# Kernel optimization log

Measured on AMD Instinct MI355X. Metric: run time of the kernel, lower is better.

Reference implementation:

```python
import jax, jax.numpy as jnp
import numpy as np
from functools import partial

H = 64  # hidden_size
F = 5   # num_features
ALPHA_RANK = 1.0
NEG_SLOPE = 0.2


def setup_inputs() -> dict:
    key = jax.random.key(0)
    ks = jax.random.split(key, 10)
    N, T = 4096, 512
    feature = jax.random.normal(ks[0], (N, T, F), dtype=jnp.float32)
    ret = jax.random.normal(ks[1], (N,), dtype=jnp.float32)
    mask = jax.random.bernoulli(ks[2], 0.9, (N,))
    s = 1.0 / np.sqrt(H)
    Wih = jax.random.uniform(ks[3], (4 * H, F), jnp.float32, -s, s)
    Whh = jax.random.uniform(ks[4], (4 * H, H), jnp.float32, -s, s)
    bih = jax.random.uniform(ks[5], (4 * H,), jnp.float32, -s, s)
    bhh = jax.random.uniform(ks[6], (4 * H,), jnp.float32, -s, s)
    Wd = jax.random.uniform(ks[7], (1, H), jnp.float32, -s, s)
    bd = jax.random.uniform(ks[8], (1,), jnp.float32, -s, s)
    return {"feature": feature, "ret": ret, "mask": mask,
            "Wih": Wih, "Whh": Whh, "bih": bih, "bhh": bhh,
            "Wd": Wd, "bd": bd}


def _lstm_last_h(x, Wih, Whh, bih, bhh):
    # x: [N, T, F] -> last hidden state [N, H]. PyTorch gate order: i, f, g, o.
    N = x.shape[0]
    b = bih + bhh
    # precompute input projections for all steps: [T, N, 4H]
    x_proj = jnp.einsum('ntf,gf->tng', x, Wih) + b

    def step(carry, xt):
        h, c = carry
        gates = xt + h @ Whh.T  # [N, 4H]
        i, f, g, o = jnp.split(gates, 4, axis=-1)
        i = jax.nn.sigmoid(i)
        f = jax.nn.sigmoid(f)
        g = jnp.tanh(g)
        o = jax.nn.sigmoid(o)
        c = f * c + i * g
        h = o * jnp.tanh(c)
        return (h, c), None

    h0 = jnp.zeros((N, H), x.dtype)
    c0 = jnp.zeros((N, H), x.dtype)
    (h, _), _ = jax.lax.scan(step, (h0, c0), x_proj)
    return h


def _masked_mse(pred, gt, mask):
    m = mask.astype(pred.dtype)
    return jnp.sum((pred - gt) ** 2 * m) / (jnp.sum(m) + 1e-8)


def _rank_loss(pred, gt, mask):
    m = mask.astype(pred.dtype)
    pred_diff = pred[None, :] - pred[:, None]   # [i,j] = pred[j]-pred[i]
    true_diff = gt[None, :] - gt[:, None]
    mm = m[None, :] * m[:, None]
    return jnp.mean(jax.nn.relu(-pred_diff * true_diff * mm))


def reference(feature, ret, mask, Wih, Whh, bih, bhh, Wd, bd):
    h_last = _lstm_last_h(feature, Wih, Whh, bih, bhh)          # [N, H]
    pred = jax.nn.leaky_relu(h_last @ Wd.T + bd, NEG_SLOPE)[:, 0]  # [N]
    reg_loss = _masked_mse(pred, ret, mask)
    rank_loss = _rank_loss(pred, ret, mask)
    loss = reg_loss + ALPHA_RANK * rank_loss
    return pred, loss, reg_loss, rank_loss
```

## Files before the change

kernel.cpp:

```cpp
#include <hip/hip_runtime.h>

#define NSEQ   4096
#define TSTEPS 512
#define FIN    5
#define HID    64
#define SPB    16
#define BLK    512

typedef __attribute__((ext_vector_type(8))) short bsh8;
typedef __attribute__((ext_vector_type(4))) float f32x4;
typedef __attribute__((ext_vector_type(2))) float f32x2;
typedef __attribute__((ext_vector_type(4))) int   i32x4;

#define MFMA16(A, B, C) __builtin_amdgcn_mfma_f32_16x16x32_bf16((A), (B), (C), 0, 0, 0)

#define LOG2E 1.4426950408889634f
#define SNEG  (-LOG2E)
#define SPOS  (2.0f * LOG2E)

struct Frag2 { bsh8 hi; bsh8 lo; };

__device__ __forceinline__ unsigned short bf16hi_rn(float x) {
    unsigned u = __float_as_uint(x);
    return (unsigned short)((u + 0x7fffu + ((u >> 16) & 1u)) >> 16);
}
__device__ __forceinline__ void split_bf16(float v, unsigned short& h, unsigned short& l) {
    h = bf16hi_rn(v);
    float hf_ = __uint_as_float(((unsigned)h) << 16);
    l = bf16hi_rn(v - hf_);
}

__device__ __forceinline__ Frag2 load_whh_frag(const float* __restrict__ Whh, int row, int k, float scale) {
    const float* p = Whh + row * HID + k;
    Frag2 r;
#pragma unroll
    for (int j = 0; j < 8; ++j) {
        unsigned short h, l;
        split_bf16(scale * p[j], h, l);
        r.hi[j] = (short)h; r.lo[j] = (short)l;
    }
    return r;
}
__device__ __forceinline__ Frag2 load_wih_frag(const float* __restrict__ Wih,
                                               const float* __restrict__ bih,
                                               const float* __restrict__ bhh,
                                               int row, int quad, float scale) {
    Frag2 r;
#pragma unroll
    for (int j = 0; j < 8; ++j) { r.hi[j] = 0; r.lo[j] = 0; }
    if (quad == 0) {
        unsigned short h, l;
#pragma unroll
        for (int j = 0; j < FIN; ++j) {
            split_bf16(scale * Wih[row * FIN + j], h, l);
            r.hi[j] = (short)h; r.lo[j] = (short)l;
        }
        split_bf16(scale * (bih[row] + bhh[row]), h, l);
        r.hi[FIN] = (short)h; r.lo[FIN] = (short)l;
    }
    return r;
}

__device__ __forceinline__ void stage_chunk(const float* __restrict__ feat,
                                            bsh8 (*dst)[SPB],
                                            int seq0, int t0, int tidE) {
#pragma unroll
    for (int it = 0; it < (64 * SPB) / 256; ++it) {
        int idx = tidE + it * 256;
        int t2  = idx >> 4;
        int s   = idx & 15;
        const float* xp = feat + (size_t)(seq0 + s) * (TSTEPS * FIN) + (t0 + t2) * FIN;
        bsh8 v = {0, 0, 0, 0, 0, 0, 0, 0};
#pragma unroll
        for (int j = 0; j < FIN; ++j) v[j] = (short)bf16hi_rn(xp[j]);
        v[FIN] = (short)0x3F80;
        dst[t2][s] = v;
    }
}

__device__ __forceinline__ void epi2(float zi0, float zf0, float zg0, float zo0,
                                     float zi1, float zf1, float zg1, float zo1,
                                     float& cs0, float& cs1, float& h0, float& h1) {
    float Ei0 = __builtin_amdgcn_exp2f(zi0), Ei1 = __builtin_amdgcn_exp2f(zi1);
    float Ef0 = __builtin_amdgcn_exp2f(zf0), Ef1 = __builtin_amdgcn_exp2f(zf1);
    float Eg0 = __builtin_amdgcn_exp2f(zg0), Eg1 = __builtin_amdgcn_exp2f(zg1);
    float P10 = (1.0f + Ei0) * (1.0f + Eg0), Pf0 = 1.0f + Ef0;
    float P11 = (1.0f + Ei1) * (1.0f + Eg1), Pf1 = 1.0f + Ef1;
    float D0 = P10 * Pf0, D1 = P11 * Pf1;
    float Rp = __builtin_amdgcn_rcpf(D0 * D1);
    float n10 = __builtin_fmaf(SPOS, Eg0, -SPOS);
    float n11 = __builtin_fmaf(SPOS, Eg1, -SPOS);
    float m0 = __builtin_fmaf(P10, cs0, n10 * Pf0);
    float m1 = __builtin_fmaf(P11, cs1, n11 * Pf1);
    cs0 = (Rp * D1) * m0;
    cs1 = (Rp * D0) * m1;
    float Eo0 = __builtin_amdgcn_exp2f(zo0), Eo1 = __builtin_amdgcn_exp2f(zo1);
    float Ec0 = __builtin_amdgcn_exp2f(cs0), Ec1 = __builtin_amdgcn_exp2f(cs1);
    float D20 = (1.0f + Eo0) * (1.0f + Ec0);
    float D21 = (1.0f + Eo1) * (1.0f + Ec1);
    float R2p = __builtin_amdgcn_rcpf(D20 * D21);
    h0 = (Ec0 - 1.0f) * (R2p * D21);
    h1 = (Ec1 - 1.0f) * (R2p * D20);
}

__global__ __launch_bounds__(BLK)
void lstm_kernel(const float* __restrict__ feat,
                 const float* __restrict__ Wih,
                 const float* __restrict__ Whh,
                 const float* __restrict__ bih,
                 const float* __restrict__ bhh,
                 const float* __restrict__ Wd,
                 const float* __restrict__ bd,
                 float* __restrict__ pred,
                 float* __restrict__ accums) {
    __shared__ bsh8  aA[2][SPB][9];
    __shared__ bsh8  xb[2][64][SPB];
    __shared__ __align__(8) f32x2 sg[2][4][4][64];
    __shared__ __align__(8) f32x2 mb[4][4][64];
    __shared__ float hf[SPB][HID + 1];
    __shared__ float pf[SPB][17];

    const int tid   = threadIdx.x;
    const int w     = tid >> 6;
    const int lane  = tid & 63;
    const int col   = lane & 15;
    const int quad  = lane >> 4;
    const int quad4 = quad * 4;
    const int seq0  = blockIdx.x * SPB;

    if (blockIdx.x == 0 && tid < 4) accums[tid] = 0.0f;

    {
        bsh8 z = {0, 0, 0, 0, 0, 0, 0, 0};
        if (tid < SPB * 9) (&aA[0][0][0])[tid] = z;
    }
    if (w >= 4) stage_chunk(feat, xb[0], seq0, 0, tid - 256);
    __syncthreads();

    if (w < 4) {
        const int u = 16 * w + col;
        const Frag2 b00 = load_whh_frag(Whh, 0*HID + u,      quad*8, SNEG);
        const Frag2 b01 = load_whh_frag(Whh, 0*HID + u, 32 + quad*8, SNEG);
        const Frag2 b10 = load_whh_frag(Whh, 1*HID + u,      quad*8, SNEG);
        const Frag2 b11 = load_whh_frag(Whh, 1*HID + u, 32 + quad*8, SNEG);
        const Frag2 b20 = load_whh_frag(Whh, 2*HID + u,      quad*8, SPOS);
        const Frag2 b21 = load_whh_frag(Whh, 2*HID + u, 32 + quad*8, SPOS);
        const Frag2 b30 = load_whh_frag(Whh, 3*HID + u,      quad*8, SNEG);
        const Frag2 b31 = load_whh_frag(Whh, 3*HID + u, 32 + quad*8, SNEG);

        float cs0 = 0.f, cs1 = 0.f;
        unsigned short* const aAb = (unsigned short*)&aA[0][0][0];
        const int rowbase = quad4 * 72 + u;
        const int aAhalf  = SPB * 9 * 8;

        for (int t = 0; t < TSTEPS; ++t) {
            const int buf = t & 1;
            const int nb  = buf ^ 1;
            __builtin_amdgcn_s_setprio(1);
            __syncthreads();

            bsh8 ah0 = aA[buf][col][quad];
            bsh8 ah1 = aA[buf][col][4 + quad];
            f32x2 s0 = sg[buf][w][0][lane];
            f32x2 s1 = sg[buf][w][1][lane];
            f32x2 s2 = sg[buf][w][2][lane];
            f32x2 s3 = sg[buf][w][3][lane];

            const f32x4 zz = {0.f, 0.f, 0.f, 0.f};
            f32x4 acc0 = MFMA16(ah0, b00.hi, zz);
            f32x4 acc1 = MFMA16(ah0, b10.hi, zz);
            f32x4 acc2 = MFMA16(ah0, b20.hi, zz);
            f32x4 acc3 = MFMA16(ah0, b30.hi, zz);
            acc0 = MFMA16(ah1, b01.hi, acc0);
            acc1 = MFMA16(ah1, b11.hi, acc1);
            acc2 = MFMA16(ah1, b21.hi, acc2);
            acc3 = MFMA16(ah1, b31.hi, acc3);
            acc0 = MFMA16(ah0, b00.lo, acc0);
            acc1 = MFMA16(ah0, b10.lo, acc1);
            acc2 = MFMA16(ah0, b20.lo, acc2);
            acc3 = MFMA16(ah0, b30.lo, acc3);
            acc0 = MFMA16(ah1, b01.lo, acc0);
            acc1 = MFMA16(ah1, b11.lo, acc1);
            acc2 = MFMA16(ah1, b21.lo, acc2);
            acc3 = MFMA16(ah1, b31.lo, acc3);

            mb[w][0][lane] = (f32x2){acc0[2], acc0[3]};
            mb[w][1][lane] = (f32x2){acc1[2], acc1[3]};
            mb[w][2][lane] = (f32x2){acc2[2], acc2[3]};
            mb[w][3][lane] = (f32x2){acc3[2], acc3[3]};
            __builtin_amdgcn_s_setprio(0);
            __syncthreads();

            float h0, h1;
            epi2(acc0[0] + s0.x, acc1[0] + s1.x, acc2[0] + s2.x, acc3[0] + s3.x,
                 acc0[1] + s0.y, acc1[1] + s1.y, acc2[1] + s2.y, acc3[1] + s3.y,
                 cs0, cs1, h0, h1);
            unsigned pk;
            asm("v_cvt_pk_bf16_f32 %0, %1, %2" : "=v"(pk) : "v"(h0), "v"(h1));
            unsigned short* hp = aAb + nb * aAhalf + rowbase;
            hp[0]  = (unsigned short)pk;
            hp[72] = (unsigned short)(pk >> 16);
            if (t == TSTEPS - 1) {
                hf[quad4 + 0][u] = h0;
                hf[quad4 + 1][u] = h1;
            }
        }
    } else {
        const int wE   = w - 4;
        const int tidE = tid - 256;
        const int uE   = 16 * wE + col;
        const Frag2 w0 = load_wih_frag(Wih, bih, bhh, 0*HID + uE, quad, SNEG);
        const Frag2 w1 = load_wih_frag(Wih, bih, bhh, 1*HID + uE, quad, SNEG);
        const Frag2 w2 = load_wih_frag(Wih, bih, bhh, 2*HID + uE, quad, SPOS);
        const Frag2 w3 = load_wih_frag(Wih, bih, bhh, 3*HID + uE, quad, SNEG);

        float cs2 = 0.f, cs3 = 0.f;
        f32x2 ps0, ps1, ps2, ps3;
        unsigned short* const aAb = (unsigned short*)&aA[0][0][0];
        const int rowbase = (quad4 + 2) * 72 + uE;
        const int aAhalf  = SPB * 9 * 8;

        {
            bsh8 ax = xb[0][0][col];
            f32x4 e0 = {0.f,0.f,0.f,0.f}, e1 = e0, e2 = e0, e3 = e0;
            e0 = MFMA16(ax, w0.hi, e0); e0 = MFMA16(ax, w0.lo, e0);
            e1 = MFMA16(ax, w1.hi, e1); e1 = MFMA16(ax, w1.lo, e1);
            e2 = MFMA16(ax, w2.hi, e2); e2 = MFMA16(ax, w2.lo, e2);
            e3 = MFMA16(ax, w3.hi, e3); e3 = MFMA16(ax, w3.lo, e3);
            sg[0][wE][0][lane] = (f32x2){e0[0], e0[1]};
            sg[0][wE][1][lane] = (f32x2){e1[0], e1[1]};
            sg[0][wE][2][lane] = (f32x2){e2[0], e2[1]};
            sg[0][wE][3][lane] = (f32x2){e3[0], e3[1]};
            ps0 = (f32x2){e0[2], e0[3]};
            ps1 = (f32x2){e1[2], e1[3]};
            ps2 = (f32x2){e2[2], e2[3]};
            ps3 = (f32x2){e3[2], e3[3]};
        }

        for (int t = 0; t < TSTEPS; ++t) {
            const int nb = (t & 1) ^ 1;
            __syncthreads();
            f32x2 ns0, ns1, ns2, ns3;
            bool have_ns = (t + 1 < TSTEPS);
            if ((t & 63) == 0 && t + 64 < TSTEPS)
                stage_chunk(feat, xb[((t >> 6) + 1) & 1], seq0, ((t >> 6) + 1) * 64, tidE);
            if (have_ns) {
                const int t1 = t + 1;
                bsh8 ax = xb[(t1 >> 6) & 1][t1 & 63][col];
                f32x4 e0 = {0.f,0.f,0.f,0.f}, e1 = e0, e2 = e0, e3 = e0;
                e0 = MFMA16(ax, w0.hi, e0); e0 = MFMA16(ax, w0.lo, e0);
                e1 = MFMA16(ax, w1.hi, e1); e1 = MFMA16(ax, w1.lo, e1);
                e2 = MFMA16(ax, w2.hi, e2); e2 = MFMA16(ax, w2.lo, e2);
                e3 = MFMA16(ax, w3.hi, e3); e3 = MFMA16(ax, w3.lo, e3);
                sg[nb][wE][0][lane] = (f32x2){e0[0], e0[1]};
                sg[nb][wE][1][lane] = (f32x2){e1[0], e1[1]};
                sg[nb][wE][2][lane] = (f32x2){e2[0], e2[1]};
                sg[nb][wE][3][lane] = (f32x2){e3[0], e3[1]};
                ns0 = (f32x2){e0[2], e0[3]};
                ns1 = (f32x2){e1[2], e1[3]};
                ns2 = (f32x2){e2[2], e2[3]};
                ns3 = (f32x2){e3[2], e3[3]};
            }
            __syncthreads();

            f32x2 m0 = mb[wE][0][lane];
            f32x2 m1 = mb[wE][1][lane];
            f32x2 m2 = mb[wE][2][lane];
            f32x2 m3 = mb[wE][3][lane];
            float h2, h3;
            epi2(m0.x + ps0.x, m1.x + ps1.x, m2.x + ps2.x, m3.x + ps3.x,
                 m0.y + ps0.y, m1.y + ps1.y, m2.y + ps2.y, m3.y + ps3.y,
                 cs2, cs3, h2, h3);
            unsigned pk;
            asm("v_cvt_pk_bf16_f32 %0, %1, %2" : "=v"(pk) : "v"(h2), "v"(h3));
            unsigned short* hp = aAb + nb * aAhalf + rowbase;
            hp[0]  = (unsigned short)pk;
            hp[72] = (unsigned short)(pk >> 16);
            if (have_ns) { ps0 = ns0; ps1 = ns1; ps2 = ns2; ps3 = ns3; }
            else {
                hf[quad4 + 2][uE] = h2;
                hf[quad4 + 3][uE] = h3;
            }
        }
    }
    __syncthreads();

    if (tid < 256) {
        int s  = tid & 15;
        int hq = tid >> 4;
        int j0 = hq * 4;
        float part = hf[s][j0] * Wd[j0] + hf[s][j0 + 1] * Wd[j0 + 1]
                   + hf[s][j0 + 2] * Wd[j0 + 2] + hf[s][j0 + 3] * Wd[j0 + 3];
        pf[s][hq] = part;
    }
    __syncthreads();
    if (tid < SPB) {
        float sum = bd[0];
#pragma unroll
        for (int j = 0; j < 16; ++j) sum += pf[tid][j];
        float p = (sum >= 0.0f) ? sum : 0.2f * sum;
        pred[seq0 + tid] = p;
    }
}

__global__ __launch_bounds__(256)
void loss_kernel(const float* __restrict__ pred,
                 const float* __restrict__ ret,
                 const int* __restrict__ mask,
                 float* __restrict__ accums) {
    __shared__ __align__(16) float sp[NSEQ];
    __shared__ __align__(16) float sg_[NSEQ];
    __shared__ __align__(16) float sq[NSEQ];
    __shared__ float wsum[8];
    int tid = threadIdx.x;
    for (int idx = tid; idx < NSEQ / 4; idx += 256) {
        f32x4 p4 = ((const f32x4*)pred)[idx];
        f32x4 g4 = ((const f32x4*)ret)[idx];
        i32x4 m4 = ((const i32x4*)mask)[idx];
        f32x4 q4;
#pragma unroll
        for (int l = 0; l < 4; ++l) q4[l] = m4[l] ? 1.0f : 0.0f;
        *(f32x4*)&sp[idx * 4] = p4;
        *(f32x4*)&sg_[idx * 4] = g4;
        *(f32x4*)&sq[idx * 4] = q4;
    }
    __syncthreads();

    if (blockIdx.x == 0) {
        float v = 0.0f, m = 0.0f;
        for (int j = tid; j < NSEQ; j += 256) {
            float mj = sq[j];
            float d  = sp[j] - sg_[j];
            v += d * d * mj;
            m += mj;
        }
#pragma unroll
        for (int off = 32; off > 0; off >>= 1) {
            v += __shfl_down(v, off, 64);
            m += __shfl_down(m, off, 64);
        }
        if ((tid & 63) == 0) {
            atomicAdd(&accums[0], v);
            atomicAdd(&accums[1], m);
        }
    }

    int iloc = tid >> 5;
    int jp   = tid & 31;
    int i    = blockIdx.x * 8 + iloc;
    float pi = sp[i], gi = sg_[i], qi = sq[i];
    float sum = 0.0f;
    for (int j0 = jp * 4; j0 < NSEQ; j0 += 128) {
        f32x4 p4 = *(const f32x4*)&sp[j0];
        f32x4 g4 = *(const f32x4*)&sg_[j0];
        f32x4 q4 = *(const f32x4*)&sq[j0];
#pragma unroll
        for (int l = 0; l < 4; ++l) {
            float t = -(p4[l] - pi) * (g4[l] - gi);
            sum += fmaxf(t, 0.0f) * q4[l];
        }
    }
    sum *= qi;
#pragma unroll
    for (int off = 16; off > 0; off >>= 1) sum += __shfl_down(sum, off, 32);
    if (jp == 0) wsum[iloc] = sum;
    __syncthreads();
    if (tid == 0) {
        float s = wsum[0] + wsum[1] + wsum[2] + wsum[3]
                + wsum[4] + wsum[5] + wsum[6] + wsum[7];
        atomicAdd(&accums[2], s);
    }
}

__global__ void final_kernel(const float* __restrict__ accums,
                             float* __restrict__ out) {
    float reg  = accums[0] / (accums[1] + 1e-8f);
    float rank = accums[2] / 16777216.0f;
    out[NSEQ + 0] = reg + rank;
    out[NSEQ + 1] = reg;
    out[NSEQ + 2] = rank;
}

extern "C" void kernel_launch(void* const* d_in, const int* in_sizes, int n_in,
                              void* d_out, int out_size, void* d_ws, size_t ws_size,
                              hipStream_t stream) {
    const float* feat = (const float*)d_in[0];
    const float* ret  = (const float*)d_in[1];
    const int*   mask = (const int*)d_in[2];
    const float* Wih  = (const float*)d_in[3];
    const float* Whh  = (const float*)d_in[4];
    const float* bih  = (const float*)d_in[5];
    const float* bhh  = (const float*)d_in[6];
    const float* Wd   = (const float*)d_in[7];
    const float* bd   = (const float*)d_in[8];
    float* out    = (float*)d_out;
    float* accums = (float*)d_ws;

    lstm_kernel<<<NSEQ / SPB, BLK, 0, stream>>>(feat, Wih, Whh, bih, bhh,
                                                Wd, bd, out, accums);
    loss_kernel<<<NSEQ / 8, 256, 0, stream>>>(out, ret, mask, accums);
    final_kernel<<<1, 1, 0, stream>>>(accums, out);
}
```

Measured before the change: 412.3 us.

## Merge producer and recurrent waves to halve per-step barriers via redundant MFMA

Replaces the warp-specialised split, where four waves ran the recurrent MFMAs and four ran input projection plus half the gate epilogue, with a uniform scheme. Every wave now computes the full recurrent and input-projection MFMAs redundantly and keeps only its half of the output rows. This removes the sg/mb LDS exchange buffers and one __syncthreads per time step, shortening the serial critical path of the recurrence. The cost is roughly double the MFMA work per SIMD, and the s_setprio hints are dropped.

```diff
diff --git a/kernel.cpp b/kernel.cpp
--- a/kernel.cpp
+++ b/kernel.cpp
@@ -63,10 +63,10 @@
 
 __device__ __forceinline__ void stage_chunk(const float* __restrict__ feat,
                                             bsh8 (*dst)[SPB],
-                                            int seq0, int t0, int tidE) {
-#pragma unroll
-    for (int it = 0; it < (64 * SPB) / 256; ++it) {
-        int idx = tidE + it * 256;
+                                            int seq0, int t0, int tid) {
+#pragma unroll
+    for (int it = 0; it < (64 * SPB) / BLK; ++it) {
+        int idx = tid + it * BLK;
         int t2  = idx >> 4;
         int s   = idx & 15;
         const float* xp = feat + (size_t)(seq0 + s) * (TSTEPS * FIN) + (t0 + t2) * FIN;
@@ -115,8 +115,6 @@
                  float* __restrict__ accums) {
     __shared__ bsh8  aA[2][SPB][9];
     __shared__ bsh8  xb[2][64][SPB];
-    __shared__ __align__(8) f32x2 sg[2][4][4][64];
-    __shared__ __align__(8) f32x2 mb[4][4][64];
     __shared__ float hf[SPB][HID + 1];
     __shared__ float pf[SPB][17];
 
@@ -126,6 +124,10 @@
     const int col   = lane & 15;
     const int quad  = lane >> 4;
     const int quad4 = quad * 4;
+    const int wg    = w & 3;
+    const int half  = w >> 2;
+    const int u     = 16 * wg + col;
+    const int r0    = quad4 + 2 * half;
     const int seq0  = blockIdx.x * SPB;
 
     if (blockIdx.x == 0 && tid < 4) accums[tid] = 0.0f;
@@ -134,153 +136,103 @@
         bsh8 z = {0, 0, 0, 0, 0, 0, 0, 0};
         if (tid < SPB * 9) (&aA[0][0][0])[tid] = z;
     }
-    if (w >= 4) stage_chunk(feat, xb[0], seq0, 0, tid - 256);
-    __syncthreads();
-
-    if (w < 4) {
-        const int u = 16 * w + col;
-        const Frag2 b00 = load_whh_frag(Whh, 0*HID + u,      quad*8, SNEG);
-        const Frag2 b01 = load_whh_frag(Whh, 0*HID + u, 32 + quad*8, SNEG);
-        const Frag2 b10 = load_whh_frag(Whh, 1*HID + u,      quad*8, SNEG);
-        const Frag2 b11 = load_whh_frag(Whh, 1*HID + u, 32 + quad*8, SNEG);
-        const Frag2 b20 = load_whh_frag(Whh, 2*HID + u,      quad*8, SPOS);
-        const Frag2 b21 = load_whh_frag(Whh, 2*HID + u, 32 + quad*8, SPOS);
-        const Frag2 b30 = load_whh_frag(Whh, 3*HID + u,      quad*8, SNEG);
-        const Frag2 b31 = load_whh_frag(Whh, 3*HID + u, 32 + quad*8, SNEG);
-
-        float cs0 = 0.f, cs1 = 0.f;
-        unsigned short* const aAb = (unsigned short*)&aA[0][0][0];
-        const int rowbase = quad4 * 72 + u;
-        const int aAhalf  = SPB * 9 * 8;
-
-        for (int t = 0; t < TSTEPS; ++t) {
-            const int buf = t & 1;
-            const int nb  = buf ^ 1;
-            __builtin_amdgcn_s_setprio(1);
-            __syncthreads();
-
-            bsh8 ah0 = aA[buf][col][quad];
-            bsh8 ah1 = aA[buf][col][4 + quad];
-            f32x2 s0 = sg[buf][w][0][lane];
-            f32x2 s1 = sg[buf][w][1][lane];
-            f32x2 s2 = sg[buf][w][2][lane];
-            f32x2 s3 = sg[buf][w][3][lane];
-
-            const f32x4 zz = {0.f, 0.f, 0.f, 0.f};
-            f32x4 acc0 = MFMA16(ah0, b00.hi, zz);
-            f32x4 acc1 = MFMA16(ah0, b10.hi, zz);
-            f32x4 acc2 = MFMA16(ah0, b20.hi, zz);
-            f32x4 acc3 = MFMA16(ah0, b30.hi, zz);
-            acc0 = MFMA16(ah1, b01.hi, acc0);
-            acc1 = MFMA16(ah1, b11.hi, acc1);
-            acc2 = MFMA16(ah1, b21.hi, acc2);
-            acc3 = MFMA16(ah1, b31.hi, acc3);
-            acc0 = MFMA16(ah0, b00.lo, acc0);
-            acc1 = MFMA16(ah0, b10.lo, acc1);
-            acc2 = MFMA16(ah0, b20.lo, acc2);
-            acc3 = MFMA16(ah0, b30.lo, acc3);
-            acc0 = MFMA16(ah1, b01.lo, acc0);
-            acc1 = MFMA16(ah1, b11.lo, acc1);
-            acc2 = MFMA16(ah1, b21.lo, acc2);
-            acc3 = MFMA16(ah1, b31.lo, acc3);
-
-            mb[w][0][lane] = (f32x2){acc0[2], acc0[3]};
-            mb[w][1][lane] = (f32x2){acc1[2], acc1[3]};
-            mb[w][2][lane] = (f32x2){acc2[2], acc2[3]};
-            mb[w][3][lane] = (f32x2){acc3[2], acc3[3]};
-            __builtin_amdgcn_s_setprio(0);
-            __syncthreads();
-
-            float h0, h1;
-            epi2(acc0[0] + s0.x, acc1[0] + s1.x, acc2[0] + s2.x, acc3[0] + s3.x,
-                 acc0[1] + s0.y, acc1[1] + s1.y, acc2[1] + s2.y, acc3[1] + s3.y,
-                 cs0, cs1, h0, h1);
-            unsigned pk;
-            asm("v_cvt_pk_bf16_f32 %0, %1, %2" : "=v"(pk) : "v"(h0), "v"(h1));
-            unsigned short* hp = aAb + nb * aAhalf + rowbase;
-            hp[0]  = (unsigned short)pk;
-            hp[72] = (unsigned short)(pk >> 16);
-            if (t == TSTEPS - 1) {
-                hf[quad4 + 0][u] = h0;
-                hf[quad4 + 1][u] = h1;
-            }
-        }
-    } else {
-        const int wE   = w - 4;
-        const int tidE = tid - 256;
-        const int uE   = 16 * wE + col;
-        const Frag2 w0 = load_wih_frag(Wih, bih, bhh, 0*HID + uE, quad, SNEG);
-        const Frag2 w1 = load_wih_frag(Wih, bih, bhh, 1*HID + uE, quad, SNEG);
-        const Frag2 w2 = load_wih_frag(Wih, bih, bhh, 2*HID + uE, quad, SPOS);
-        const Frag2 w3 = load_wih_frag(Wih, bih, bhh, 3*HID + uE, quad, SNEG);
-
-        float cs2 = 0.f, cs3 = 0.f;
-        f32x2 ps0, ps1, ps2, ps3;
-        unsigned short* const aAb = (unsigned short*)&aA[0][0][0];
-        const int rowbase = (quad4 + 2) * 72 + uE;
-        const int aAhalf  = SPB * 9 * 8;
-
-        {
-            bsh8 ax = xb[0][0][col];
+    stage_chunk(feat, xb[0], seq0, 0, tid);
+
+    const Frag2 b00 = load_whh_frag(Whh, 0*HID + u,      quad*8, SNEG);
+    const Frag2 b01 = load_whh_frag(Whh, 0*HID + u, 32 + quad*8, SNEG);
+    const Frag2 b10 = load_whh_frag(Whh, 1*HID + u,      quad*8, SNEG);
+    const Frag2 b11 = load_whh_frag(Whh, 1*HID + u, 32 + quad*8, SNEG);
+    const Frag2 b20 = load_whh_frag(Whh, 2*HID + u,      quad*8, SPOS);
+    const Frag2 b21 = load_whh_frag(Whh, 2*HID + u, 32 + quad*8, SPOS);
+    const Frag2 b30 = load_whh_frag(Whh, 3*HID + u,      quad*8, SNEG);
+    const Frag2 b31 = load_whh_frag(Whh, 3*HID + u, 32 + quad*8, SNEG);
+    const Frag2 w0_ = load_wih_frag(Wih, bih, bhh, 0*HID + u, quad, SNEG);
+    const Frag2 w1_ = load_wih_frag(Wih, bih, bhh, 1*HID + u, quad, SNEG);
+    const Frag2 w2_ = load_wih_frag(Wih, bih, bhh, 2*HID + u, quad, SPOS);
+    const Frag2 w3_ = load_wih_frag(Wih, bih, bhh, 3*HID + u, quad, SNEG);
+
+    __syncthreads();
+
+    float cs0 = 0.f, cs1 = 0.f;
+    f32x2 ps0, ps1, ps2, ps3;
+
+    {
+        bsh8 ax = xb[0][0][col];
+        f32x4 e0 = {0.f,0.f,0.f,0.f}, e1 = e0, e2 = e0, e3 = e0;
+        e0 = MFMA16(ax, w0_.hi, e0); e0 = MFMA16(ax, w0_.lo, e0);
+        e1 = MFMA16(ax, w1_.hi, e1); e1 = MFMA16(ax, w1_.lo, e1);
+        e2 = MFMA16(ax, w2_.hi, e2); e2 = MFMA16(ax, w2_.lo, e2);
+        e3 = MFMA16(ax, w3_.hi, e3); e3 = MFMA16(ax, w3_.lo, e3);
+        ps0 = half ? (f32x2){e0[2], e0[3]} : (f32x2){e0[0], e0[1]};
+        ps1 = half ? (f32x2){e1[2], e1[3]} : (f32x2){e1[0], e1[1]};
+        ps2 = half ? (f32x2){e2[2], e2[3]} : (f32x2){e2[0], e2[1]};
+        ps3 = half ? (f32x2){e3[2], e3[3]} : (f32x2){e3[0], e3[1]};
+    }
+
+    unsigned short* const aAb = (unsigned short*)&aA[0][0][0];
+    const int rowbase = r0 * 72 + u;
+    const int aAhalf  = SPB * 9 * 8;
+
+    for (int t = 0; t < TSTEPS; ++t) {
+        const int buf = t & 1;
+        const int nb  = buf ^ 1;
+        __syncthreads();
+
+        bsh8 ah0 = aA[buf][col][quad];
+        bsh8 ah1 = aA[buf][col][4 + quad];
+
+        const f32x4 zz = {0.f, 0.f, 0.f, 0.f};
+        f32x4 acc0 = MFMA16(ah0, b00.hi, zz);
+        f32x4 acc1 = MFMA16(ah0, b10.hi, zz);
+        f32x4 acc2 = MFMA16(ah0, b20.hi, zz);
+        f32x4 acc3 = MFMA16(ah0, b30.hi, zz);
+        acc0 = MFMA16(ah1, b01.hi, acc0);
+        acc1 = MFMA16(ah1, b11.hi, acc1);
+        acc2 = MFMA16(ah1, b21.hi, acc2);
+        acc3 = MFMA16(ah1, b31.hi, acc3);
+        acc0 = MFMA16(ah0, b00.lo, acc0);
+        acc1 = MFMA16(ah0, b10.lo, acc1);
+        acc2 = MFMA16(ah0, b20.lo, acc2);
+        acc3 = MFMA16(ah0, b30.lo, acc3);
+        acc0 = MFMA16(ah1, b01.lo, acc0);
+        acc1 = MFMA16(ah1, b11.lo, acc1);
+        acc2 = MFMA16(ah1, b21.lo, acc2);
+        acc3 = MFMA16(ah1, b31.lo, acc3);
+
+        float a00 = half ? acc0[2] : acc0[0], a01 = half ? acc0[3] : acc0[1];
+        float a10 = half ? acc1[2] : acc1[0], a11 = half ? acc1[3] : acc1[1];
+        float a20 = half ? acc2[2] : acc2[0], a21 = half ? acc2[3] : acc2[1];
+        float a30 = half ? acc3[2] : acc3[0], a31 = half ? acc3[3] : acc3[1];
+
+        float h0, h1;
+        epi2(a00 + ps0.x, a10 + ps1.x, a20 + ps2.x, a30 + ps3.x,
+             a01 + ps0.y, a11 + ps1.y, a21 + ps2.y, a31 + ps3.y,
+             cs0, cs1, h0, h1);
+
+        unsigned pk;
+        asm("v_cvt_pk_bf16_f32 %0, %1, %2" : "=v"(pk) : "v"(h0), "v"(h1));
+        unsigned short* hp = aAb + nb * aAhalf + rowbase;
+        hp[0]  = (unsigned short)pk;
+        hp[72] = (unsigned short)(pk >> 16);
+        if (t == TSTEPS - 1) {
+            hf[r0 + 0][u] = h0;
+            hf[r0 + 1][u] = h1;
+        }
+
+        if ((t & 63) == 0 && t + 64 < TSTEPS)
+            stage_chunk(feat, xb[((t >> 6) + 1) & 1], seq0, ((t >> 6) + 1) * 64, tid);
+        if (t + 1 < TSTEPS) {
+            const int t1 = t + 1;
+            bsh8 ax = xb[(t1 >> 6) & 1][t1 & 63][col];
             f32x4 e0 = {0.f,0.f,0.f,0.f}, e1 = e0, e2 = e0, e3 = e0;
-            e0 = MFMA16(ax, w0.hi, e0); e0 = MFMA16(ax, w0.lo, e0);
-            e1 = MFMA16(ax, w1.hi, e1); e1 = MFMA16(ax, w1.lo, e1);
-            e2 = MFMA16(ax, w2.hi, e2); e2 = MFMA16(ax, w2.lo, e2);
-            e3 = MFMA16(ax, w3.hi, e3); e3 = MFMA16(ax, w3.lo, e3);
-            sg[0][wE][0][lane] = (f32x2){e0[0], e0[1]};
-            sg[0][wE][1][lane] = (f32x2){e1[0], e1[1]};
-            sg[0][wE][2][lane] = (f32x2){e2[0], e2[1]};
-            sg[0][wE][3][lane] = (f32x2){e3[0], e3[1]};
-            ps0 = (f32x2){e0[2], e0[3]};
-            ps1 = (f32x2){e1[2], e1[3]};
-            ps2 = (f32x2){e2[2], e2[3]};
-            ps3 = (f32x2){e3[2], e3[3]};
-        }
-
-        for (int t = 0; t < TSTEPS; ++t) {
-            const int nb = (t & 1) ^ 1;
-            __syncthreads();
-            f32x2 ns0, ns1, ns2, ns3;
-            bool have_ns = (t + 1 < TSTEPS);
-            if ((t & 63) == 0 && t + 64 < TSTEPS)
-                stage_chunk(feat, xb[((t >> 6) + 1) & 1], seq0, ((t >> 6) + 1) * 64, tidE);
-            if (have_ns) {
-                const int t1 = t + 1;
-                bsh8 ax = xb[(t1 >> 6) & 1][t1 & 63][col];
-                f32x4 e0 = {0.f,0.f,0.f,0.f}, e1 = e0, e2 = e0, e3 = e0;
-                e0 = MFMA16(ax, w0.hi, e0); e0 = MFMA16(ax, w0.lo, e0);
-                e1 = MFMA16(ax, w1.hi, e1); e1 = MFMA16(ax, w1.lo, e1);
-                e2 = MFMA16(ax, w2.hi, e2); e2 = MFMA16(ax, w2.lo, e2);
-                e3 = MFMA16(ax, w3.hi, e3); e3 = MFMA16(ax, w3.lo, e3);
-                sg[nb][wE][0][lane] = (f32x2){e0[0], e0[1]};
-                sg[nb][wE][1][lane] = (f32x2){e1[0], e1[1]};
-                sg[nb][wE][2][lane] = (f32x2){e2[0], e2[1]};
-                sg[nb][wE][3][lane] = (f32x2){e3[0], e3[1]};
-                ns0 = (f32x2){e0[2], e0[3]};
-                ns1 = (f32x2){e1[2], e1[3]};
-                ns2 = (f32x2){e2[2], e2[3]};
-                ns3 = (f32x2){e3[2], e3[3]};
-            }
-            __syncthreads();
-
-            f32x2 m0 = mb[wE][0][lane];
-            f32x2 m1 = mb[wE][1][lane];
-            f32x2 m2 = mb[wE][2][lane];
-            f32x2 m3 = mb[wE][3][lane];
-            float h2, h3;
-            epi2(m0.x + ps0.x, m1.x + ps1.x, m2.x + ps2.x, m3.x + ps3.x,
-                 m0.y + ps0.y, m1.y + ps1.y, m2.y + ps2.y, m3.y + ps3.y,
-                 cs2, cs3, h2, h3);
-            unsigned pk;
-            asm("v_cvt_pk_bf16_f32 %0, %1, %2" : "=v"(pk) : "v"(h2), "v"(h3));
-            unsigned short* hp = aAb + nb * aAhalf + rowbase;
-            hp[0]  = (unsigned short)pk;
-            hp[72] = (unsigned short)(pk >> 16);
-            if (have_ns) { ps0 = ns0; ps1 = ns1; ps2 = ns2; ps3 = ns3; }
-            else {
-                hf[quad4 + 2][uE] = h2;
-                hf[quad4 + 3][uE] = h3;
-            }
+            e0 = MFMA16(ax, w0_.hi, e0); e0 = MFMA16(ax, w0_.lo, e0);
+            e1 = MFMA16(ax, w1_.hi, e1); e1 = MFMA16(ax, w1_.lo, e1);
+            e2 = MFMA16(ax, w2_.hi, e2); e2 = MFMA16(ax, w2_.lo, e2);
+            e3 = MFMA16(ax, w3_.hi, e3); e3 = MFMA16(ax, w3_.lo, e3);
+            ps0 = half ? (f32x2){e0[2], e0[3]} : (f32x2){e0[0], e0[1]};
+            ps1 = half ? (f32x2){e1[2], e1[3]} : (f32x2){e1[0], e1[1]};
+            ps2 = half ? (f32x2){e2[2], e2[3]} : (f32x2){e2[0], e2[1]};
+            ps3 = half ? (f32x2){e3[2], e3[3]} : (f32x2){e3[0], e3[1]};
         }
     }
     __syncthreads();
```

Result: slower. 432.7 us (+5.0%).

## Halve sequences per block and drop mid-step barrier via lane shuffles

Applied to the files above, without the earlier changes.

Sequences per block drop from 16 to 8, so there are twice as many blocks, and the MFMA tiles keep 16 columns with the unused half zero-padded. The recurrent warps now take the upper accumulator rows from the opposite half-wave with __shfl_xor and run the whole gate epilogue themselves. That removes the LDS handoff buffer, the second per-step __syncthreads, and the epilogue work the input-projection warps used to do. The cost is that half of the MFMA work computes padding, and each block now covers fewer sequences for the same per-step latency. Launch bounds now request 4 blocks to raise occupancy.

```diff
diff --git a/kernel.cpp b/kernel.cpp
--- a/kernel.cpp
+++ b/kernel.cpp
@@ -4,7 +4,7 @@
 #define TSTEPS 512
 #define FIN    5
 #define HID    64
-#define SPB    16
+#define SPB    8
 #define BLK    512
 
 typedef __attribute__((ext_vector_type(8))) short bsh8;
@@ -62,13 +62,13 @@
 }
 
 __device__ __forceinline__ void stage_chunk(const float* __restrict__ feat,
-                                            bsh8 (*dst)[SPB],
+                                            bsh8 (*dst)[16],
                                             int seq0, int t0, int tidE) {
 #pragma unroll
     for (int it = 0; it < (64 * SPB) / 256; ++it) {
         int idx = tidE + it * 256;
-        int t2  = idx >> 4;
-        int s   = idx & 15;
+        int t2  = idx >> 3;
+        int s   = idx & 7;
         const float* xp = feat + (size_t)(seq0 + s) * (TSTEPS * FIN) + (t0 + t2) * FIN;
         bsh8 v = {0, 0, 0, 0, 0, 0, 0, 0};
 #pragma unroll
@@ -103,7 +103,7 @@
     h1 = (Ec1 - 1.0f) * (R2p * D20);
 }
 
-__global__ __launch_bounds__(BLK)
+__global__ __launch_bounds__(BLK, 4)
 void lstm_kernel(const float* __restrict__ feat,
                  const float* __restrict__ Wih,
                  const float* __restrict__ Whh,
@@ -113,10 +113,9 @@
                  const float* __restrict__ bd,
                  float* __restrict__ pred,
                  float* __restrict__ accums) {
-    __shared__ bsh8  aA[2][SPB][9];
-    __shared__ bsh8  xb[2][64][SPB];
+    __shared__ bsh8  aA[2][16][9];
+    __shared__ bsh8  xb[2][64][16];
     __shared__ __align__(8) f32x2 sg[2][4][4][64];
-    __shared__ __align__(8) f32x2 mb[4][4][64];
     __shared__ float hf[SPB][HID + 1];
     __shared__ float pf[SPB][17];
 
@@ -125,17 +124,26 @@
     const int lane  = tid & 63;
     const int col   = lane & 15;
     const int quad  = lane >> 4;
-    const int quad4 = quad * 4;
     const int seq0  = blockIdx.x * SPB;
 
     if (blockIdx.x == 0 && tid < 4) accums[tid] = 0.0f;
 
     {
         bsh8 z = {0, 0, 0, 0, 0, 0, 0, 0};
-        if (tid < SPB * 9) (&aA[0][0][0])[tid] = z;
+        if (tid < 2 * 16 * 9) (&aA[0][0][0])[tid] = z;
+#pragma unroll
+        for (int k = 0; k < 2; ++k) {
+            int i  = tid + k * BLK;
+            int b  = i >> 9;
+            int t2 = (i >> 3) & 63;
+            int s8 = 8 + (i & 7);
+            xb[b][t2][s8] = z;
+        }
     }
     if (w >= 4) stage_chunk(feat, xb[0], seq0, 0, tid - 256);
-    __syncthreads();
+
+    const int rA  = (quad & 1) * 4 + ((quad >> 1) ? 2 : 0);
+    const bool loq = (quad < 2);
 
     if (w < 4) {
         const int u = 16 * w + col;
@@ -148,15 +156,17 @@
         const Frag2 b30 = load_whh_frag(Whh, 3*HID + u,      quad*8, SNEG);
         const Frag2 b31 = load_whh_frag(Whh, 3*HID + u, 32 + quad*8, SNEG);
 
+        __syncthreads();
+
         float cs0 = 0.f, cs1 = 0.f;
         unsigned short* const aAb = (unsigned short*)&aA[0][0][0];
-        const int rowbase = quad4 * 72 + u;
-        const int aAhalf  = SPB * 9 * 8;
+        const int rowbase = rA * 72 + u;
+        const int aAhalf  = 16 * 9 * 8;
+        __builtin_amdgcn_s_setprio(1);
 
         for (int t = 0; t < TSTEPS; ++t) {
             const int buf = t & 1;
             const int nb  = buf ^ 1;
-            __builtin_amdgcn_s_setprio(1);
             __syncthreads();
 
             bsh8 ah0 = aA[buf][col][quad];
@@ -184,27 +194,28 @@
             acc2 = MFMA16(ah1, b21.lo, acc2);
             acc3 = MFMA16(ah1, b31.lo, acc3);
 
-            mb[w][0][lane] = (f32x2){acc0[2], acc0[3]};
-            mb[w][1][lane] = (f32x2){acc1[2], acc1[3]};
-            mb[w][2][lane] = (f32x2){acc2[2], acc2[3]};
-            mb[w][3][lane] = (f32x2){acc3[2], acc3[3]};
-            __builtin_amdgcn_s_setprio(0);
-            __syncthreads();
+            float x00 = __shfl_xor(acc0[2], 32, 64), x01 = __shfl_xor(acc0[3], 32, 64);
+            float x10 = __shfl_xor(acc1[2], 32, 64), x11 = __shfl_xor(acc1[3], 32, 64);
+            float x20 = __shfl_xor(acc2[2], 32, 64), x21 = __shfl_xor(acc2[3], 32, 64);
+            float x30 = __shfl_xor(acc3[2], 32, 64), x31 = __shfl_xor(acc3[3], 32, 64);
+            float zi0 = (loq ? acc0[0] : x00) + s0.x, zi1 = (loq ? acc0[1] : x01) + s0.y;
+            float zf0 = (loq ? acc1[0] : x10) + s1.x, zf1 = (loq ? acc1[1] : x11) + s1.y;
+            float zg0 = (loq ? acc2[0] : x20) + s2.x, zg1 = (loq ? acc2[1] : x21) + s2.y;
+            float zo0 = (loq ? acc3[0] : x30) + s3.x, zo1 = (loq ? acc3[1] : x31) + s3.y;
 
             float h0, h1;
-            epi2(acc0[0] + s0.x, acc1[0] + s1.x, acc2[0] + s2.x, acc3[0] + s3.x,
-                 acc0[1] + s0.y, acc1[1] + s1.y, acc2[1] + s2.y, acc3[1] + s3.y,
-                 cs0, cs1, h0, h1);
+            epi2(zi0, zf0, zg0, zo0, zi1, zf1, zg1, zo1, cs0, cs1, h0, h1);
             unsigned pk;
             asm("v_cvt_pk_bf16_f32 %0, %1, %2" : "=v"(pk) : "v"(h0), "v"(h1));
             unsigned short* hp = aAb + nb * aAhalf + rowbase;
             hp[0]  = (unsigned short)pk;
             hp[72] = (unsigned short)(pk >> 16);
             if (t == TSTEPS - 1) {
-                hf[quad4 + 0][u] = h0;
-                hf[quad4 + 1][u] = h1;
+                hf[rA + 0][u] = h0;
+                hf[rA + 1][u] = h1;
             }
         }
+        __builtin_amdgcn_s_setprio(0);
     } else {
         const int wE   = w - 4;
         const int tidE = tid - 256;
@@ -214,11 +225,7 @@
         const Frag2 w2 = load_wih_frag(Wih, bih, bhh, 2*HID + uE, quad, SPOS);
         const Frag2 w3 = load_wih_frag(Wih, bih, bhh, 3*HID + uE, quad, SNEG);
 
-        float cs2 = 0.f, cs3 = 0.f;
-        f32x2 ps0, ps1, ps2, ps3;
-        unsigned short* const aAb = (unsigned short*)&aA[0][0][0];
-        const int rowbase = (quad4 + 2) * 72 + uE;
-        const int aAhalf  = SPB * 9 * 8;
+        __syncthreads();
 
         {
             bsh8 ax = xb[0][0][col];
@@ -227,24 +234,20 @@
             e1 = MFMA16(ax, w1.hi, e1); e1 = MFMA16(ax, w1.lo, e1);
             e2 = MFMA16(ax, w2.hi, e2); e2 = MFMA16(ax, w2.lo, e2);
             e3 = MFMA16(ax, w3.hi, e3); e3 = MFMA16(ax, w3.lo, e3);
-            sg[0][wE][0][lane] = (f32x2){e0[0], e0[1]};
-            sg[0][wE][1][lane] = (f32x2){e1[0], e1[1]};
-            sg[0][wE][2][lane] = (f32x2){e2[0], e2[1]};
-            sg[0][wE][3][lane] = (f32x2){e3[0], e3[1]};
-            ps0 = (f32x2){e0[2], e0[3]};
-            ps1 = (f32x2){e1[2], e1[3]};
-            ps2 = (f32x2){e2[2], e2[3]};
-            ps3 = (f32x2){e3[2], e3[3]};
-        }
-
+            float x0 = __shfl_xor(e0[2], 32, 64), x0b = __shfl_xor(e0[3], 32, 64);
+            float x1 = __shfl_xor(e1[2], 32, 64), x1b = __shfl_xor(e1[3], 32, 64);
+            float x2 = __shfl_xor(e2[2], 32, 64), x2b = __shfl_xor(e2[3], 32, 64);
+            float x3 = __shfl_xor(e3[2], 32, 64), x3b = __shfl_xor(e3[3], 32, 64);
+            sg[0][wE][0][lane] = (f32x2){loq ? e0[0] : x0, loq ? e0[1] : x0b};
+            sg[0][wE][1][lane] = (f32x2){loq ? e1[0] : x1, loq ? e1[1] : x1b};
+            sg[0][wE][2][lane] = (f32x2){loq ? e2[0] : x2, loq ? e2[1] : x2b};
+            sg[0][wE][3][lane] = (f32x2){loq ? e3[0] : x3, loq ? e3[1] : x3b};
+        }
         for (int t = 0; t < TSTEPS; ++t) {
-            const int nb = (t & 1) ^ 1;
             __syncthreads();
-            f32x2 ns0, ns1, ns2, ns3;
-            bool have_ns = (t + 1 < TSTEPS);
             if ((t & 63) == 0 && t + 64 < TSTEPS)
                 stage_chunk(feat, xb[((t >> 6) + 1) & 1], seq0, ((t >> 6) + 1) * 64, tidE);
-            if (have_ns) {
+            if (t + 1 < TSTEPS) {
                 const int t1 = t + 1;
                 bsh8 ax = xb[(t1 >> 6) & 1][t1 & 63][col];
                 f32x4 e0 = {0.f,0.f,0.f,0.f}, e1 = e0, e2 = e0, e3 = e0;
@@ -252,42 +255,23 @@
                 e1 = MFMA16(ax, w1.hi, e1); e1 = MFMA16(ax, w1.lo, e1);
                 e2 = MFMA16(ax, w2.hi, e2); e2 = MFMA16(ax, w2.lo, e2);
                 e3 = MFMA16(ax, w3.hi, e3); e3 = MFMA16(ax, w3.lo, e3);
-                sg[nb][wE][0][lane] = (f32x2){e0[0], e0[1]};
-                sg[nb][wE][1][lane] = (f32x2){e1[0], e1[1]};
-                sg[nb][wE][2][lane] = (f32x2){e2[0], e2[1]};
-                sg[nb][wE][3][lane] = (f32x2){e3[0], e3[1]};
-                ns0 = (f32x2){e0[2], e0[3]};
-                ns1 = (f32x2){e1[2], e1[3]};
-                ns2 = (f32x2){e2[2], e2[3]};
-                ns3 = (f32x2){e3[2], e3[3]};
+                float x0 = __shfl_xor(e0[2], 32, 64), x0b = __shfl_xor(e0[3], 32, 64);
+                float x1 = __shfl_xor(e1[2], 32, 64), x1b = __shfl_xor(e1[3], 32, 64);
+                float x2 = __shfl_xor(e2[2], 32, 64), x2b = __shfl_xor(e2[3], 32, 64);
+                float x3 = __shfl_xor(e3[2], 32, 64), x3b = __shfl_xor(e3[3], 32, 64);
+                const int sb = t1 & 1;
+                sg[sb][wE][0][lane] = (f32x2){loq ? e0[0] : x0, loq ? e0[1] : x0b};
+                sg[sb][wE][1][lane] = (f32x2){loq ? e1[0] : x1, loq ? e1[1] : x1b};
+                sg[sb][wE][2][lane] = (f32x2){loq ? e2[0] : x2, loq ? e2[1] : x2b};
+                sg[sb][wE][3][lane] = (f32x2){loq ? e3[0] : x3, loq ? e3[1] : x3b};
             }
-            __syncthreads();
-
-            f32x2 m0 = mb[wE][0][lane];
-            f32x2 m1 = mb[wE][1][lane];
-            f32x2 m2 = mb[wE][2][lane];
-            f32x2 m3 = mb[wE][3][lane];
-            float h2, h3;
-            epi2(m0.x + ps0.x, m1.x + ps1.x, m2.x + ps2.x, m3.x + ps3.x,
-                 m0.y + ps0.y, m1.y + ps1.y, m2.y + ps2.y, m3.y + ps3.y,
-                 cs2, cs3, h2, h3);
-            unsigned pk;
-            asm("v_cvt_pk_bf16_f32 %0, %1, %2" : "=v"(pk) : "v"(h2), "v"(h3));
-            unsigned short* hp = aAb + nb * aAhalf + rowbase;
-            hp[0]  = (unsigned short)pk;
-            hp[72] = (unsigned short)(pk >> 16);
-            if (have_ns) { ps0 = ns0; ps1 = ns1; ps2 = ns2; ps3 = ns3; }
-            else {
-                hf[quad4 + 2][uE] = h2;
-                hf[quad4 + 3][uE] = h3;
-            }
         }
     }
     __syncthreads();
 
-    if (tid < 256) {
-        int s  = tid & 15;
-        int hq = tid >> 4;
+    if (tid < 8 * 16) {
+        int s  = tid & 7;
+        int hq = tid >> 3;
         int j0 = hq * 4;
         float part = hf[s][j0] * Wd[j0] + hf[s][j0 + 1] * Wd[j0 + 1]
                    + hf[s][j0 + 2] * Wd[j0 + 2] + hf[s][j0 + 3] * Wd[j0 + 3];
```

Result: slower. 467.0 us (+13.3%).
